# Kernel tuning notes

Hardware: AMD Instinct MI355X
Metric: run time of the kernel (lower is better)

The kernel has to match this reference:

```python
import jax, jax.numpy as jnp
import numpy as np

B, A, C, H, W = 16, 5, 512, 16, 16


def _affine_grid(theta, Hh, Ww):
    # torch F.affine_grid, align_corners=False (default). theta: [2,3]
    xs = (2.0 * jnp.arange(Ww, dtype=jnp.float32) + 1.0) / Ww - 1.0  # [W]
    ys = (2.0 * jnp.arange(Hh, dtype=jnp.float32) + 1.0) / Hh - 1.0  # [H]
    gx = theta[0, 0] * xs[None, :] + theta[0, 1] * ys[:, None] + theta[0, 2]  # [H,W]
    gy = theta[1, 0] * xs[None, :] + theta[1, 1] * ys[:, None] + theta[1, 2]  # [H,W]
    return gx, gy


def _grid_sample(img, gx, gy):
    # torch F.grid_sample, bilinear, padding_mode='zeros', align_corners=False
    # img: [C,H,W]; gx,gy: [H,W] normalized coords
    C_, Hh, Ww = img.shape
    ix = ((gx + 1.0) * Ww - 1.0) * 0.5
    iy = ((gy + 1.0) * Hh - 1.0) * 0.5
    x0 = jnp.floor(ix); y0 = jnp.floor(iy)
    x1 = x0 + 1.0;      y1 = y0 + 1.0
    wx1 = ix - x0; wx0 = 1.0 - wx1
    wy1 = iy - y0; wy0 = 1.0 - wy1

    def gather(xi, yi):
        inb = (xi >= 0) & (xi < Ww) & (yi >= 0) & (yi < Hh)
        xc = jnp.clip(xi, 0, Ww - 1).astype(jnp.int32)
        yc = jnp.clip(yi, 0, Hh - 1).astype(jnp.int32)
        return img[:, yc, xc] * inb[None].astype(img.dtype)  # [C,H,W]

    return (gather(x0, y0) * (wx0 * wy0)[None] + gather(x1, y0) * (wx1 * wy0)[None]
          + gather(x0, y1) * (wx0 * wy1)[None] + gather(x1, y1) * (wx1 * wy1)[None])


def _warp(nb_feat, nb_warp):
    # nb_feat: [C,H,W] neighbor feature; nb_warp: [4,4] pose matrix
    zero = jnp.zeros((), dtype=jnp.float32)
    one = jnp.ones((), dtype=jnp.float32)
    theta_rot = jnp.stack([
        jnp.stack([nb_warp[0, 0], nb_warp[0, 1], zero]),
        jnp.stack([nb_warp[1, 0], nb_warp[1, 1], zero])])  # [2,3]
    gx_r, gy_r = _affine_grid(theta_rot, H, W)
    feat_rot = _grid_sample(nb_feat, gx_r, gy_r)
    x_trans = 4.0 * nb_warp[0, 3] / 128.0
    y_trans = -(4.0 * nb_warp[1, 3]) / 128.0
    theta_trans = jnp.stack([
        jnp.stack([one, zero, x_trans]),
        jnp.stack([zero, one, y_trans])])
    gx_t, gy_t = _affine_grid(theta_trans, H, W)
    return _grid_sample(feat_rot, gx_t, gy_t)  # [C,H,W]


def _fuse_one(local_b, trans_b, n):
    # local_b: [A,C,H,W], trans_b: [A,A,4,4], n: scalar num_agent
    # pair[i,j] = warp of agent j's feature into agent i's frame
    pair = jax.vmap(lambda t_i: jax.vmap(_warp)(local_b, t_i))(trans_b)  # [A,A,C,H,W]
    idx = jnp.arange(A)
    mask = (idx[:, None] != idx[None, :]) & (idx[:, None] < n) & (idx[None, :] < n)
    return local_b + jnp.einsum('ij,ijchw->ichw', mask.astype(local_b.dtype), pair)


def setup_inputs() -> dict:
    key = jax.random.key(0)
    k1, k2, k3, k4 = jax.random.split(key, 4)
    feat_maps = jax.random.normal(k1, (A * B, C, H, W), dtype=jnp.float32)
    # realistic near-rigid pose matrices: rotation block + translation column
    ang = jax.random.uniform(k2, (B, A, A), minval=-0.5, maxval=0.5)
    tr = jax.random.normal(k3, (B, A, A, 2), dtype=jnp.float32) * 8.0
    tm = jnp.zeros((B, A, A, 4, 4), dtype=jnp.float32)
    tm = tm.at[..., 0, 0].set(jnp.cos(ang)).at[..., 0, 1].set(-jnp.sin(ang))
    tm = tm.at[..., 1, 0].set(jnp.sin(ang)).at[..., 1, 1].set(jnp.cos(ang))
    tm = tm.at[..., 0, 3].set(tr[..., 0]).at[..., 1, 3].set(tr[..., 1])
    tm = tm.at[..., 2, 2].set(1.0).at[..., 3, 3].set(1.0)
    num_agent = jax.random.randint(k4, (B, A), 1, 6, dtype=jnp.int64) if jax.config.jax_enable_x64 else jax.random.randint(k4, (B, A), 1, 6, dtype=jnp.int32)
    return {"feat_maps": feat_maps, "trans_matrices": tm, "num_agent_tensor": num_agent}


def reference(feat_maps, trans_matrices, num_agent_tensor):
    # feat_maps is agent-major blocks of size B (feat_maps[B*i:B*(i+1)] is agent i)
    local = feat_maps.reshape(A, B, C, H, W).transpose(1, 0, 2, 3, 4)  # [B,A,C,H,W]
    fused = jax.vmap(_fuse_one)(local, trans_matrices, num_agent_tensor[:, 0])
    # agents2batch: concat agents along batch dim -> [A*B,C,H,W]
    return fused.transpose(1, 0, 2, 3, 4).reshape(A * B, C, H, W)
```

## Files before the change

### kernel.cpp

```cpp
#include <hip/hip_runtime.h>

#define NB 16
#define NA 5
#define NC 512
#define HW 256
#define NBLK 2048
#define NTOT 5120

typedef float f4 __attribute__((ext_vector_type(4)));
typedef _Float16 h8 __attribute__((ext_vector_type(8)));

static __device__ __forceinline__ h8 splat8(float v) {
    const _Float16 h = (_Float16)v;
    h8 r = {h, h, h, h, h, h, h, h};
    return r;
}

static __device__ __forceinline__ h8 rot_sample2(const h8* __restrict__ src,
        float xA, float yA, float wA,
        float xB, float yB, float wB) {
    const float fxA = floorf(xA), fyA = floorf(yA);
    const float fxB = floorf(xB), fyB = floorf(yB);
    const int ixA = (int)fxA, iyA = (int)fyA;
    const int ixB = (int)fxB, iyB = (int)fyB;
    const float wxA1 = xA - fxA, wyA1 = yA - fyA;
    const float wxB1 = xB - fxB, wyB1 = yB - fyB;
    const float mxA0 = (ixA     >= 0 && ixA     < 16) ? 1.0f - wxA1 : 0.0f;
    const float mxA1 = (ixA + 1 >= 0 && ixA + 1 < 16) ? wxA1 : 0.0f;
    const float myA0 = (iyA     >= 0 && iyA     < 16) ? (1.0f - wyA1) * wA : 0.0f;
    const float myA1 = (iyA + 1 >= 0 && iyA + 1 < 16) ? wyA1 * wA : 0.0f;
    const float mxB0 = (ixB     >= 0 && ixB     < 16) ? 1.0f - wxB1 : 0.0f;
    const float mxB1 = (ixB + 1 >= 0 && ixB + 1 < 16) ? wxB1 : 0.0f;
    const float myB0 = (iyB     >= 0 && iyB     < 16) ? (1.0f - wyB1) * wB : 0.0f;
    const float myB1 = (iyB + 1 >= 0 && iyB + 1 < 16) ? wyB1 * wB : 0.0f;
    const int cxA0 = min(max(ixA, 0), 15), cxA1 = min(max(ixA + 1, 0), 15);
    const int cyA0 = min(max(iyA, 0), 15), cyA1 = min(max(iyA + 1, 0), 15);
    const int cxB0 = min(max(ixB, 0), 15), cxB1 = min(max(ixB + 1, 0), 15);
    const int cyB0 = min(max(iyB, 0), 15), cyB1 = min(max(iyB + 1, 0), 15);
    const h8 vA00 = src[cyA0 * 16 + cxA0];
    const h8 vA01 = src[cyA0 * 16 + cxA1];
    const h8 vA10 = src[cyA1 * 16 + cxA0];
    const h8 vA11 = src[cyA1 * 16 + cxA1];
    const h8 vB00 = src[cyB0 * 16 + cxB0];
    const h8 vB01 = src[cyB0 * 16 + cxB1];
    const h8 vB10 = src[cyB1 * 16 + cxB0];
    const h8 vB11 = src[cyB1 * 16 + cxB1];
    return (vA00 * splat8(mxA0) + vA01 * splat8(mxA1)) * splat8(myA0)
         + (vA10 * splat8(mxA0) + vA11 * splat8(mxA1)) * splat8(myA1)
         + (vB00 * splat8(mxB0) + vB01 * splat8(mxB1)) * splat8(myB0)
         + (vB10 * splat8(mxB0) + vB11 * splat8(mxB1)) * splat8(myB1);
}

struct Item {
    int i, b, c0, n;
    bool work;
    float own[8];
    float nb[4][8];
    f4 r0[4], r1[4];
};

static __device__ __forceinline__ Item prefetch_item(
        const float* __restrict__ feat, const float* __restrict__ trans,
        const int* __restrict__ numa, int idx, int p) {
    Item it;
    const int g = idx & 63;
    const int r = idx >> 6;
    it.i = r % NA;
    it.b = r / NA;
    it.c0 = g << 3;
    it.n = numa[it.b * NA];
    it.work = (it.i < it.n) && (it.n > 1);
    const float* own = feat + ((it.i * NB + it.b) * NC + it.c0) * HW + p;
#pragma unroll
    for (int k = 0; k < 8; ++k) it.own[k] = own[k * HW];
    if (it.work) {
#pragma unroll
        for (int jj = 0; jj < 4; ++jj) {
            const int j = jj + (jj >= it.i);
            if (j < it.n) {
                const f4* tw = (const f4*)(trans + (((it.b * NA) + it.i) * NA + j) * 16);
                it.r0[jj] = tw[0];
                it.r1[jj] = tw[1];
                const float* src = feat + ((j * NB + it.b) * NC + it.c0) * HW + p;
#pragma unroll
                for (int k = 0; k < 8; ++k) it.nb[jj][k] = src[k * HW];
            }
        }
    }
    return it;
}

__global__ __launch_bounds__(256) void fafmimo_pipe_kernel(
    const float* __restrict__ feat,
    const float* __restrict__ trans,
    const int*   __restrict__ numa,
    float*       __restrict__ out)
{
    __shared__ h8 lds_nb[4][HW];

    const int p = threadIdx.x;
    const int x = p & 15, y = p >> 4;
    bool dirty = false;

    int idx = blockIdx.x;
    Item cur = prefetch_item(feat, trans, numa, idx, p);

    while (true) {
        if (cur.work) {
            if (dirty) __syncthreads();
#pragma unroll
            for (int jj = 0; jj < 4; ++jj) {
                const int j = jj + (jj >= cur.i);
                if (j < cur.n) {
                    h8 v;
#pragma unroll
                    for (int k = 0; k < 8; ++k) v[k] = (_Float16)cur.nb[jj][k];
                    lds_nb[jj][p] = v;
                }
            }
            __syncthreads();
            dirty = true;
        }

        const int nidx = idx + NBLK;
        const bool more = nidx < NTOT;
        Item nxt;
        if (more) nxt = prefetch_item(feat, trans, numa, nidx, p);

        float acc[8];
#pragma unroll
        for (int k = 0; k < 8; ++k) acc[k] = cur.own[k];

        if (cur.work) {
            h8 pair_acc = splat8(0.0f);
#pragma unroll
            for (int jj = 0; jj < 4; ++jj) {
                const int j = jj + (jj >= cur.i);
                if (j < cur.n) {
                    const float r00 = cur.r0[jj].x, r01 = cur.r0[jj].y;
                    const float r10 = cur.r1[jj].x, r11 = cur.r1[jj].y;

                    const float dx = 0.25f * cur.r0[jj].w;
                    const float dy = -0.25f * cur.r1[jj].w;
                    const float fdx = floorf(dx), fdy = floorf(dy);
                    const float tx1 = dx - fdx, tx0 = 1.0f - tx1;
                    const float ty1 = dy - fdy, ty0 = 1.0f - ty1;
                    const int ox = x + (int)fdx;
                    const int oy = y + (int)fdy;
                    const bool inx0 = (ox >= 0) && (ox < 16);
                    const bool inx1 = (ox + 1 >= 0) && (ox + 1 < 16);
                    const bool iny0 = (oy >= 0) && (oy < 16);
                    const bool iny1 = (oy + 1 >= 0) && (oy + 1 < 16);
                    const float ws00 = (inx0 && iny0) ? tx0 * ty0 : 0.0f;
                    const float ws10 = (inx1 && iny0) ? tx1 * ty0 : 0.0f;
                    const float ws01 = (inx0 && iny1) ? tx0 * ty1 : 0.0f;
                    const float ws11 = (inx1 && iny1) ? tx1 * ty1 : 0.0f;

                    const float fox = (float)ox - 7.5f;
                    const float foy = (float)oy - 7.5f;
                    const float bxr = r00 * fox + r01 * foy + 7.5f;
                    const float byr = r10 * fox + r11 * foy + 7.5f;

                    const h8* srcj = &lds_nb[jj][0];
                    pair_acc += rot_sample2(srcj,
                        bxr,       byr,       ws00,
                        bxr + r00, byr + r10, ws10);
                    pair_acc += rot_sample2(srcj,
                        bxr + r01,       byr + r11,       ws01,
                        bxr + r00 + r01, byr + r10 + r11, ws11);
                }
            }
#pragma unroll
            for (int k = 0; k < 8; ++k) acc[k] += (float)pair_acc[k];
        }

        float* dst = out + ((cur.i * NB + cur.b) * NC + cur.c0) * HW + p;
#pragma unroll
        for (int k = 0; k < 8; ++k) dst[k * HW] = acc[k];

        if (!more) break;
        cur = nxt;
        idx = nidx;
    }
}

extern "C" void kernel_launch(void* const* d_in, const int* in_sizes, int n_in,
                              void* d_out, int out_size, void* d_ws, size_t ws_size,
                              hipStream_t stream) {
    const float* feat  = (const float*)d_in[0];
    const float* trans = (const float*)d_in[1];
    const int*   numa  = (const int*)d_in[2];
    float* out = (float*)d_out;

    fafmimo_pipe_kernel<<<dim3(NBLK), dim3(256), 0, stream>>>(
        feat, trans, numa, out);
}
```

Baseline: 100.1 us.

## Split warp into two LDS-staged phases: rotate, then translate

The kernel no longer evaluates the rotation sample at all four translation taps, which took 16 gathers per neighbour. It now does two passes. First each thread computes its rotated pixel and writes it to a second LDS buffer, then after a barrier it does a 4-tap translation gather from that buffer. This cuts the LDS reads and bilinear arithmetic per neighbour by about four times. In exchange it doubles LDS use, adds a barrier per item and raises the occupancy hint in launch_bounds to 4. Transform scalars are also forced uniform with readfirstlane so they can live in scalar registers.

```diff
diff --git a/kernel.cpp b/kernel.cpp
--- a/kernel.cpp
+++ b/kernel.cpp
@@ -7,7 +7,6 @@
 #define NBLK 2048
 #define NTOT 5120
 
-typedef float f4 __attribute__((ext_vector_type(4)));
 typedef _Float16 h8 __attribute__((ext_vector_type(8)));
 
 static __device__ __forceinline__ h8 splat8(float v) {
@@ -16,39 +15,9 @@
     return r;
 }
 
-static __device__ __forceinline__ h8 rot_sample2(const h8* __restrict__ src,
-        float xA, float yA, float wA,
-        float xB, float yB, float wB) {
-    const float fxA = floorf(xA), fyA = floorf(yA);
-    const float fxB = floorf(xB), fyB = floorf(yB);
-    const int ixA = (int)fxA, iyA = (int)fyA;
-    const int ixB = (int)fxB, iyB = (int)fyB;
-    const float wxA1 = xA - fxA, wyA1 = yA - fyA;
-    const float wxB1 = xB - fxB, wyB1 = yB - fyB;
-    const float mxA0 = (ixA     >= 0 && ixA     < 16) ? 1.0f - wxA1 : 0.0f;
-    const float mxA1 = (ixA + 1 >= 0 && ixA + 1 < 16) ? wxA1 : 0.0f;
-    const float myA0 = (iyA     >= 0 && iyA     < 16) ? (1.0f - wyA1) * wA : 0.0f;
-    const float myA1 = (iyA + 1 >= 0 && iyA + 1 < 16) ? wyA1 * wA : 0.0f;
-    const float mxB0 = (ixB     >= 0 && ixB     < 16) ? 1.0f - wxB1 : 0.0f;
-    const float mxB1 = (ixB + 1 >= 0 && ixB + 1 < 16) ? wxB1 : 0.0f;
-    const float myB0 = (iyB     >= 0 && iyB     < 16) ? (1.0f - wyB1) * wB : 0.0f;
-    const float myB1 = (iyB + 1 >= 0 && iyB + 1 < 16) ? wyB1 * wB : 0.0f;
-    const int cxA0 = min(max(ixA, 0), 15), cxA1 = min(max(ixA + 1, 0), 15);
-    const int cyA0 = min(max(iyA, 0), 15), cyA1 = min(max(iyA + 1, 0), 15);
-    const int cxB0 = min(max(ixB, 0), 15), cxB1 = min(max(ixB + 1, 0), 15);
-    const int cyB0 = min(max(iyB, 0), 15), cyB1 = min(max(iyB + 1, 0), 15);
-    const h8 vA00 = src[cyA0 * 16 + cxA0];
-    const h8 vA01 = src[cyA0 * 16 + cxA1];
-    const h8 vA10 = src[cyA1 * 16 + cxA0];
-    const h8 vA11 = src[cyA1 * 16 + cxA1];
-    const h8 vB00 = src[cyB0 * 16 + cxB0];
-    const h8 vB01 = src[cyB0 * 16 + cxB1];
-    const h8 vB10 = src[cyB1 * 16 + cxB0];
-    const h8 vB11 = src[cyB1 * 16 + cxB1];
-    return (vA00 * splat8(mxA0) + vA01 * splat8(mxA1)) * splat8(myA0)
-         + (vA10 * splat8(mxA0) + vA11 * splat8(mxA1)) * splat8(myA1)
-         + (vB00 * splat8(mxB0) + vB01 * splat8(mxB1)) * splat8(myB0)
-         + (vB10 * splat8(mxB0) + vB11 * splat8(mxB1)) * splat8(myB1);
+static __device__ __forceinline__ float rfl(float v) {
+    return __builtin_bit_cast(float,
+        __builtin_amdgcn_readfirstlane(__builtin_bit_cast(int, v)));
 }
 
 struct Item {
@@ -56,7 +25,7 @@
     bool work;
     float own[8];
     float nb[4][8];
-    f4 r0[4], r1[4];
+    float tr[4][6];
 };
 
 static __device__ __forceinline__ Item prefetch_item(
@@ -78,9 +47,13 @@
         for (int jj = 0; jj < 4; ++jj) {
             const int j = jj + (jj >= it.i);
             if (j < it.n) {
-                const f4* tw = (const f4*)(trans + (((it.b * NA) + it.i) * NA + j) * 16);
-                it.r0[jj] = tw[0];
-                it.r1[jj] = tw[1];
+                const float* tw = trans + (((it.b * NA) + it.i) * NA + j) * 16;
+                it.tr[jj][0] = rfl(tw[0]);
+                it.tr[jj][1] = rfl(tw[1]);
+                it.tr[jj][2] = rfl(tw[3]);
+                it.tr[jj][3] = rfl(tw[4]);
+                it.tr[jj][4] = rfl(tw[5]);
+                it.tr[jj][5] = rfl(tw[7]);
                 const float* src = feat + ((j * NB + it.b) * NC + it.c0) * HW + p;
 #pragma unroll
                 for (int k = 0; k < 8; ++k) it.nb[jj][k] = src[k * HW];
@@ -90,16 +63,19 @@
     return it;
 }
 
-__global__ __launch_bounds__(256) void fafmimo_pipe_kernel(
+__global__ __launch_bounds__(256, 4) void fafmimo_twophase_kernel(
     const float* __restrict__ feat,
     const float* __restrict__ trans,
     const int*   __restrict__ numa,
     float*       __restrict__ out)
 {
     __shared__ h8 lds_nb[4][HW];
+    __shared__ h8 lds_rot[4][HW];
 
     const int p = threadIdx.x;
     const int x = p & 15, y = p >> 4;
+    const float fx = (float)x - 7.5f;
+    const float fy = (float)y - 7.5f;
     bool dirty = false;
 
     int idx = blockIdx.x;
@@ -132,46 +108,63 @@
         for (int k = 0; k < 8; ++k) acc[k] = cur.own[k];
 
         if (cur.work) {
-            h8 pair_acc = splat8(0.0f);
 #pragma unroll
             for (int jj = 0; jj < 4; ++jj) {
                 const int j = jj + (jj >= cur.i);
                 if (j < cur.n) {
-                    const float r00 = cur.r0[jj].x, r01 = cur.r0[jj].y;
-                    const float r10 = cur.r1[jj].x, r11 = cur.r1[jj].y;
+                    const float bx = cur.tr[jj][0] * fx + cur.tr[jj][1] * fy + 7.5f;
+                    const float by = cur.tr[jj][3] * fx + cur.tr[jj][4] * fy + 7.5f;
+                    const float fbx = floorf(bx), fby = floorf(by);
+                    const int ix = (int)fbx, iy = (int)fby;
+                    const float wx1 = bx - fbx, wy1 = by - fby;
+                    const float mx0 = (ix     >= 0 && ix     < 16) ? 1.0f - wx1 : 0.0f;
+                    const float mx1 = (ix + 1 >= 0 && ix + 1 < 16) ? wx1 : 0.0f;
+                    const float my0 = (iy     >= 0 && iy     < 16) ? 1.0f - wy1 : 0.0f;
+                    const float my1 = (iy + 1 >= 0 && iy + 1 < 16) ? wy1 : 0.0f;
+                    const int cx0 = min(max(ix, 0), 15), cx1 = min(max(ix + 1, 0), 15);
+                    const int cy0 = min(max(iy, 0), 15), cy1 = min(max(iy + 1, 0), 15);
+                    const h8 v00 = lds_nb[jj][cy0 * 16 + cx0];
+                    const h8 v01 = lds_nb[jj][cy0 * 16 + cx1];
+                    const h8 v10 = lds_nb[jj][cy1 * 16 + cx0];
+                    const h8 v11 = lds_nb[jj][cy1 * 16 + cx1];
+                    lds_rot[jj][p] =
+                          v00 * splat8(mx0 * my0) + v01 * splat8(mx1 * my0)
+                        + v10 * splat8(mx0 * my1) + v11 * splat8(mx1 * my1);
+                }
+            }
+            __syncthreads();
 
-                    const float dx = 0.25f * cur.r0[jj].w;
-                    const float dy = -0.25f * cur.r1[jj].w;
+#pragma unroll
+            for (int jj = 0; jj < 4; ++jj) {
+                const int j = jj + (jj >= cur.i);
+                if (j < cur.n) {
+                    const float dx = 0.25f * cur.tr[jj][2];
+                    const float dy = -0.25f * cur.tr[jj][5];
                     const float fdx = floorf(dx), fdy = floorf(dy);
                     const float tx1 = dx - fdx, tx0 = 1.0f - tx1;
                     const float ty1 = dy - fdy, ty0 = 1.0f - ty1;
                     const int ox = x + (int)fdx;
                     const int oy = y + (int)fdy;
-                    const bool inx0 = (ox >= 0) && (ox < 16);
+                    const bool inx0 = (ox     >= 0) && (ox     < 16);
                     const bool inx1 = (ox + 1 >= 0) && (ox + 1 < 16);
-                    const bool iny0 = (oy >= 0) && (oy < 16);
+                    const bool iny0 = (oy     >= 0) && (oy     < 16);
                     const bool iny1 = (oy + 1 >= 0) && (oy + 1 < 16);
-                    const float ws00 = (inx0 && iny0) ? tx0 * ty0 : 0.0f;
-                    const float ws10 = (inx1 && iny0) ? tx1 * ty0 : 0.0f;
-                    const float ws01 = (inx0 && iny1) ? tx0 * ty1 : 0.0f;
-                    const float ws11 = (inx1 && iny1) ? tx1 * ty1 : 0.0f;
-
-                    const float fox = (float)ox - 7.5f;
-                    const float foy = (float)oy - 7.5f;
-                    const float bxr = r00 * fox + r01 * foy + 7.5f;
-                    const float byr = r10 * fox + r11 * foy + 7.5f;
-
-                    const h8* srcj = &lds_nb[jj][0];
-                    pair_acc += rot_sample2(srcj,
-                        bxr,       byr,       ws00,
-                        bxr + r00, byr + r10, ws10);
-                    pair_acc += rot_sample2(srcj,
-                        bxr + r01,       byr + r11,       ws01,
-                        bxr + r00 + r01, byr + r10 + r11, ws11);
+                    const float w00 = (inx0 && iny0) ? tx0 * ty0 : 0.0f;
+                    const float w10 = (inx1 && iny0) ? tx1 * ty0 : 0.0f;
+                    const float w01 = (inx0 && iny1) ? tx0 * ty1 : 0.0f;
+                    const float w11 = (inx1 && iny1) ? tx1 * ty1 : 0.0f;
+                    const int cx0 = min(max(ox, 0), 15), cx1 = min(max(ox + 1, 0), 15);
+                    const int cy0 = min(max(oy, 0), 15), cy1 = min(max(oy + 1, 0), 15);
+                    const h8 t00 = lds_rot[jj][cy0 * 16 + cx0];
+                    const h8 t01 = lds_rot[jj][cy0 * 16 + cx1];
+                    const h8 t10 = lds_rot[jj][cy1 * 16 + cx0];
+                    const h8 t11 = lds_rot[jj][cy1 * 16 + cx1];
+                    const h8 s = t00 * splat8(w00) + t01 * splat8(w10)
+                               + t10 * splat8(w01) + t11 * splat8(w11);
+#pragma unroll
+                    for (int k = 0; k < 8; ++k) acc[k] += (float)s[k];
                 }
             }
-#pragma unroll
-            for (int k = 0; k < 8; ++k) acc[k] += (float)pair_acc[k];
         }
 
         float* dst = out + ((cur.i * NB + cur.b) * NC + cur.c0) * HW + p;
@@ -192,6 +185,6 @@
     const int*   numa  = (const int*)d_in[2];
     float* out = (float*)d_out;
 
-    fafmimo_pipe_kernel<<<dim3(NBLK), dim3(256), 0, stream>>>(
+    fafmimo_twophase_kernel<<<dim3(NBLK), dim3(256), 0, stream>>>(
         feat, trans, numa, out);
 }
```

After: 96.82 us. -3.3%, faster.

## Stage all agents' channels once per block and reuse across output agents

Applied to the files above, without the earlier changes.

Replaces the persistent prefetch-pipelined loop over (agent, batch, channel-group) items with one block per (batch, channel-group). The block loads all agents' features into LDS once and then computes every output agent from that shared copy. This removes the repeated neighbor loads, each of which was previously fetched up to four times. The change also reads transform scalars via readfirstlane, accumulates per-pair in fp32 instead of fp16 across pairs, and sets a launch-bounds occupancy hint. In exchange it drops the cross-item prefetch overlap and launches fewer blocks (1024), each doing serial work over five agents.

```diff
diff --git a/kernel.cpp b/kernel.cpp
--- a/kernel.cpp
+++ b/kernel.cpp
@@ -4,16 +4,18 @@
 #define NA 5
 #define NC 512
 #define HW 256
-#define NBLK 2048
-#define NTOT 5120
 
-typedef float f4 __attribute__((ext_vector_type(4)));
 typedef _Float16 h8 __attribute__((ext_vector_type(8)));
 
 static __device__ __forceinline__ h8 splat8(float v) {
     const _Float16 h = (_Float16)v;
     h8 r = {h, h, h, h, h, h, h, h};
     return r;
+}
+
+static __device__ __forceinline__ float rfl(float v) {
+    return __builtin_bit_cast(float,
+        __builtin_amdgcn_readfirstlane(__builtin_bit_cast(int, v)));
 }
 
 static __device__ __forceinline__ h8 rot_sample2(const h8* __restrict__ src,
@@ -51,105 +53,63 @@
          + (vB10 * splat8(mxB0) + vB11 * splat8(mxB1)) * splat8(myB1);
 }
 
-struct Item {
-    int i, b, c0, n;
-    bool work;
-    float own[8];
-    float nb[4][8];
-    f4 r0[4], r1[4];
-};
-
-static __device__ __forceinline__ Item prefetch_item(
-        const float* __restrict__ feat, const float* __restrict__ trans,
-        const int* __restrict__ numa, int idx, int p) {
-    Item it;
-    const int g = idx & 63;
-    const int r = idx >> 6;
-    it.i = r % NA;
-    it.b = r / NA;
-    it.c0 = g << 3;
-    it.n = numa[it.b * NA];
-    it.work = (it.i < it.n) && (it.n > 1);
-    const float* own = feat + ((it.i * NB + it.b) * NC + it.c0) * HW + p;
-#pragma unroll
-    for (int k = 0; k < 8; ++k) it.own[k] = own[k * HW];
-    if (it.work) {
-#pragma unroll
-        for (int jj = 0; jj < 4; ++jj) {
-            const int j = jj + (jj >= it.i);
-            if (j < it.n) {
-                const f4* tw = (const f4*)(trans + (((it.b * NA) + it.i) * NA + j) * 16);
-                it.r0[jj] = tw[0];
-                it.r1[jj] = tw[1];
-                const float* src = feat + ((j * NB + it.b) * NC + it.c0) * HW + p;
-#pragma unroll
-                for (int k = 0; k < 8; ++k) it.nb[jj][k] = src[k * HW];
-            }
-        }
-    }
-    return it;
-}
-
-__global__ __launch_bounds__(256) void fafmimo_pipe_kernel(
+__global__ __launch_bounds__(256, 4) void fafmimo_fused1b_kernel(
     const float* __restrict__ feat,
     const float* __restrict__ trans,
     const int*   __restrict__ numa,
     float*       __restrict__ out)
 {
-    __shared__ h8 lds_nb[4][HW];
+    __shared__ h8 lds_nb[NA][HW];
 
     const int p = threadIdx.x;
     const int x = p & 15, y = p >> 4;
-    bool dirty = false;
 
-    int idx = blockIdx.x;
-    Item cur = prefetch_item(feat, trans, numa, idx, p);
+    const int b  = blockIdx.x & 15;
+    const int c0 = (blockIdx.x >> 4) << 3;
+    const int n  = numa[b * NA];
 
-    while (true) {
-        if (cur.work) {
-            if (dirty) __syncthreads();
+#pragma unroll
+    for (int a = 0; a < NA; ++a) {
+        if (a < n) {
+            const float* src = feat + ((a * NB + b) * NC + c0) * HW + p;
+            h8 v;
+#pragma unroll
+            for (int k = 0; k < 8; ++k) v[k] = (_Float16)src[k * HW];
+            lds_nb[a][p] = v;
+        }
+    }
+    __syncthreads();
+
+#pragma unroll
+    for (int i = 0; i < NA; ++i) {
+        const float* own = feat + ((i * NB + b) * NC + c0) * HW + p;
+        float ownv[8];
+#pragma unroll
+        for (int k = 0; k < 8; ++k) ownv[k] = own[k * HW];
+
+        float psum[8];
+#pragma unroll
+        for (int k = 0; k < 8; ++k) psum[k] = 0.0f;
+
+        if (n > 1 && i < n) {
 #pragma unroll
             for (int jj = 0; jj < 4; ++jj) {
-                const int j = jj + (jj >= cur.i);
-                if (j < cur.n) {
-                    h8 v;
-#pragma unroll
-                    for (int k = 0; k < 8; ++k) v[k] = (_Float16)cur.nb[jj][k];
-                    lds_nb[jj][p] = v;
-                }
-            }
-            __syncthreads();
-            dirty = true;
-        }
+                const int j = jj + (jj >= i);
+                if (j < n) {
+                    const float* tw = trans + (((b * NA) + i) * NA + j) * 16;
+                    const float r00 = rfl(tw[0]), r01 = rfl(tw[1]);
+                    const float r10 = rfl(tw[4]), r11 = rfl(tw[5]);
 
-        const int nidx = idx + NBLK;
-        const bool more = nidx < NTOT;
-        Item nxt;
-        if (more) nxt = prefetch_item(feat, trans, numa, nidx, p);
-
-        float acc[8];
-#pragma unroll
-        for (int k = 0; k < 8; ++k) acc[k] = cur.own[k];
-
-        if (cur.work) {
-            h8 pair_acc = splat8(0.0f);
-#pragma unroll
-            for (int jj = 0; jj < 4; ++jj) {
-                const int j = jj + (jj >= cur.i);
-                if (j < cur.n) {
-                    const float r00 = cur.r0[jj].x, r01 = cur.r0[jj].y;
-                    const float r10 = cur.r1[jj].x, r11 = cur.r1[jj].y;
-
-                    const float dx = 0.25f * cur.r0[jj].w;
-                    const float dy = -0.25f * cur.r1[jj].w;
+                    const float dx =  0.25f * rfl(tw[3]);
+                    const float dy = -0.25f * rfl(tw[7]);
                     const float fdx = floorf(dx), fdy = floorf(dy);
                     const float tx1 = dx - fdx, tx0 = 1.0f - tx1;
                     const float ty1 = dy - fdy, ty0 = 1.0f - ty1;
                     const int ox = x + (int)fdx;
                     const int oy = y + (int)fdy;
-                    const bool inx0 = (ox >= 0) && (ox < 16);
+                    const bool inx0 = (ox     >= 0) && (ox     < 16);
                     const bool inx1 = (ox + 1 >= 0) && (ox + 1 < 16);
-                    const bool iny0 = (oy >= 0) && (oy < 16);
+                    const bool iny0 = (oy     >= 0) && (oy     < 16);
                     const bool iny1 = (oy + 1 >= 0) && (oy + 1 < 16);
                     const float ws00 = (inx0 && iny0) ? tx0 * ty0 : 0.0f;
                     const float ws10 = (inx1 && iny0) ? tx1 * ty0 : 0.0f;
@@ -161,26 +121,22 @@
                     const float bxr = r00 * fox + r01 * foy + 7.5f;
                     const float byr = r10 * fox + r11 * foy + 7.5f;
 
-                    const h8* srcj = &lds_nb[jj][0];
-                    pair_acc += rot_sample2(srcj,
+                    const h8* srcj = &lds_nb[j][0];
+                    h8 pair = rot_sample2(srcj,
                         bxr,       byr,       ws00,
                         bxr + r00, byr + r10, ws10);
-                    pair_acc += rot_sample2(srcj,
+                    pair   += rot_sample2(srcj,
                         bxr + r01,       byr + r11,       ws01,
                         bxr + r00 + r01, byr + r10 + r11, ws11);
+#pragma unroll
+                    for (int k = 0; k < 8; ++k) psum[k] += (float)pair[k];
                 }
             }
-#pragma unroll
-            for (int k = 0; k < 8; ++k) acc[k] += (float)pair_acc[k];
         }
 
-        float* dst = out + ((cur.i * NB + cur.b) * NC + cur.c0) * HW + p;
+        float* dst = out + ((i * NB + b) * NC + c0) * HW + p;
 #pragma unroll
-        for (int k = 0; k < 8; ++k) dst[k * HW] = acc[k];
-
-        if (!more) break;
-        cur = nxt;
-        idx = nidx;
+        for (int k = 0; k < 8; ++k) dst[k * HW] = ownv[k] + psum[k];
     }
 }
 
@@ -192,6 +148,6 @@
     const int*   numa  = (const int*)d_in[2];
     float* out = (float*)d_out;
 
-    fafmimo_pipe_kernel<<<dim3(NBLK), dim3(256), 0, stream>>>(
+    fafmimo_fused1b_kernel<<<dim3(NB * 64), dim3(256), 0, stream>>>(
         feat, trans, numa, out);
 }
```

New measurement: 178.6 us. 1.78x slower.
